# Kernel tuning notes

Measured on AMD Instinct MI355X. Metric: run time of the kernel, lower is better.

## Reference

```python
import jax, jax.numpy as jnp
import numpy as np
from jax import lax

B, CI, CO, H, W = 32, 64, 64, 128, 128
NUM_EXPERTS = 5
NUM_TASKS = 10  # num_tasks=9 + 1 internal global task
K = 5


def setup_inputs() -> dict:
    key = jax.random.key(0)
    ks = jax.random.split(key, 9)
    # kaiming_uniform_ with a=sqrt(5), fan_out -> bound = sqrt(6/((1+5)*fan_out))
    def kaiming(k, co, ci, ksz):
        fan_out = co * ksz * ksz
        bound = np.sqrt(6.0 / (6.0 * fan_out))
        return jax.random.uniform(k, (co, ci, ksz, ksz), jnp.float32, -bound, bound)
    gw_bound = 1.0 / np.sqrt(NUM_TASKS)
    return {
        "x": jax.random.normal(ks[0], (B, CI, H, W), jnp.float32),
        "task_id": jax.random.randint(ks[1], (B,), 0, NUM_TASKS),
        "gate_w": jax.random.uniform(ks[2], (NUM_EXPERTS * CO, NUM_TASKS), jnp.float32, -gw_bound, gw_bound),
        "gate_b": jax.random.uniform(ks[3], (NUM_EXPERTS * CO,), jnp.float32, -gw_bound, gw_bound),
        "w5": kaiming(ks[4], CO, CI, 5),
        "w3": kaiming(ks[5], CO, CI, 3),
        "w1": kaiming(ks[6], CO, CI, 1),
        "wavg3": kaiming(ks[7], CO, CI, 1),
        "wavg5": kaiming(ks[8], CO, CI, 1),
    }


def _expert_bank(w5, w3, w1, wavg3, wavg5):
    # All experts expressed as 5x5 kernels, stacked: [E, O, I, 5, 5]
    pad = lambda w, p: jnp.pad(w, ((0, 0), (0, 0), (p, p), (p, p)))
    avg3 = jnp.full((3, 3), 1.0 / 9.0, w5.dtype)
    avg5 = jnp.full((5, 5), 1.0 / 25.0, w5.dtype)
    e_conv5 = w5
    e_conv3 = pad(w3, 1)
    e_conv1 = pad(w1, 2)
    e_avg3 = pad(wavg3 * avg3[None, None], 1)  # [O,I,1,1]*[3,3] broadcast
    e_avg5 = wavg5 * avg5[None, None]
    return jnp.stack([e_conv5, e_conv3, e_conv1, e_avg3, e_avg5])


def reference(x, task_id, gate_w, gate_b, w5, w3, w1, wavg3, wavg5):
    # Gate: one-hot task -> per-(expert, out_channel) routing weights
    t = jax.nn.one_hot(task_id, NUM_TASKS, dtype=x.dtype)          # [B, T]
    g = t @ gate_w.T + gate_b                                       # [B, E*O]
    g = jax.nn.softmax(g.reshape(-1, NUM_EXPERTS, CO), axis=1)      # [B, E, O]

    experts = _expert_bank(w5, w3, w1, wavg3, wavg5)                # [E, O, I, 5, 5]
    # Batched kernel synthesis (replaces per-sample python loop of einsums)
    w = jnp.einsum('eoikl,beo->boikl', experts, g)                  # [B, O, I, 5, 5]

    # Per-sample conv2d, stride 1, 'same' padding
    def conv1(xi, wi):
        return lax.conv_general_dilated(
            xi[None], wi, (1, 1), 'SAME',
            dimension_numbers=('NCHW', 'OIHW', 'NCHW'))[0]
    y = jax.vmap(conv1)(x, w)                                       # [B, O, H, W]
    # conv_type='final' -> Identity subsequent layer; eval mode -> task_id unchanged
    return y, task_id
```

## Files before the change

kernel.cpp:

```cpp
#include <hip/hip_runtime.h>

#define WK_OFFSET_BYTES 71368704ull

using bf16x8   = __attribute__((ext_vector_type(8)))  __bf16;
using floatx16 = __attribute__((ext_vector_type(16))) float;

static __device__ __forceinline__ unsigned short f2bf(float f) {
    unsigned int u = __float_as_uint(f);
    u += 0x7FFFu + ((u >> 16) & 1u);
    return (unsigned short)(u >> 16);
}

static __device__ __forceinline__ floatx16 mfma16(bf16x8 a, bf16x8 b, floatx16 c) {
    return __builtin_amdgcn_mfma_f32_32x32x16_bf16(a, b, c, 0, 0, 0);
}

static __device__ __forceinline__ void gload_lds16(const void* g, void* l) {
    __builtin_amdgcn_global_load_lds(
        (const __attribute__((address_space(1))) void*)g,
        (__attribute__((address_space(3))) void*)l, 16, 0, 0);
}

__global__ __launch_bounds__(256) void pre_kernel(
    const float* __restrict__ x,
    const float* __restrict__ gate_w, const float* __restrict__ gate_b,
    const float* __restrict__ w5, const float* __restrict__ w3,
    const float* __restrict__ w1, const float* __restrict__ wavg3,
    const float* __restrict__ wavg5, const int* __restrict__ task_id,
    unsigned short* __restrict__ xt, unsigned short* __restrict__ wk,
    float* __restrict__ out_task)
{
    const int blk = blockIdx.x;
    const int tid = threadIdx.x;
    __shared__ float g[5][64];

    if (blk < 4224) {
        const int b  = blk / 132;
        const int hp = blk - b * 132;
        const int h  = hp - 2;
        const bool vrow = (h >= 0) && (h < 128);
        unsigned short* dst_row = xt + (size_t)blk * 8448;

        for (int i = tid; i < 1056; i += 256) {
            int cc = i / 132;
            int wp = i - cc * 132;
            unsigned int pk[4] = {0u, 0u, 0u, 0u};
            if (vrow && wp >= 2 && wp < 130) {
                const float* xp = x + (((size_t)(b * 64 + cc * 8) * 128 + h) * 128 + (wp - 2));
                #pragma unroll
                for (int j = 0; j < 4; ++j) {
                    unsigned short lo = f2bf(xp[(2 * j)     * 16384]);
                    unsigned short hi = f2bf(xp[(2 * j + 1) * 16384]);
                    pk[j] = (unsigned int)lo | ((unsigned int)hi << 16);
                }
            }
            *(uint4*)(dst_row + (size_t)i * 8) = make_uint4(pk[0], pk[1], pk[2], pk[3]);
        }
    } else {
        const int pb = blk - 4224;
        const int t = pb >> 4;
        const int chunk = pb & 15;

        if (tid < 64) {
            float l[5];
            float m = -1e30f;
            #pragma unroll
            for (int e = 0; e < 5; ++e) {
                l[e] = gate_w[(e * 64 + tid) * 10 + t] + gate_b[e * 64 + tid];
                m = fmaxf(m, l[e]);
            }
            float s = 0.f;
            #pragma unroll
            for (int e = 0; e < 5; ++e) { l[e] = expf(l[e] - m); s += l[e]; }
            float inv = 1.f / s;
            #pragma unroll
            for (int e = 0; e < 5; ++e) g[e][tid] = l[e] * inv;
        }
        __syncthreads();

        for (int it = 0; it < 25; ++it) {
            int idx = chunk * 6400 + it * 256 + tid;
            int ci  = idx & 63;
            int o   = (idx >> 6) & 63;
            int tap = idx >> 12;
            int ky = tap / 5, kx = tap - ky * 5;

            float v = g[0][o] * w5[(o * 64 + ci) * 25 + tap];
            bool in3 = (ky >= 1 && ky <= 3 && kx >= 1 && kx <= 3);
            if (in3) {
                v += g[1][o] * w3[(o * 64 + ci) * 9 + (ky - 1) * 3 + (kx - 1)];
                v += g[3][o] * wavg3[o * 64 + ci] * (1.f / 9.f);
            }
            if (ky == 2 && kx == 2) v += g[2][o] * w1[o * 64 + ci];
            v += g[4][o] * wavg5[o * 64 + ci] * (1.f / 25.f);

            wk[(t * 25 + tap) * 4096 + o * 64 + ci] = f2bf(v);
        }

        if (pb == 0 && tid < 32) out_task[tid] = (float)task_id[tid];
    }
}

__global__ __launch_bounds__(512, 2) void conv_kernel(
    const unsigned short* __restrict__ xt, const unsigned short* __restrict__ wk,
    const int* __restrict__ task_id, float* __restrict__ out)
{
    __shared__ unsigned short ibuf[2][25344];
    __shared__ unsigned short wlds[25600];

    const int blk = ((blockIdx.x & 7) << 6) | (blockIdx.x >> 3);
    const int b  = blk >> 4;
    const int ht = blk & 15;
    const int t  = task_id[b];

    const int tid  = threadIdx.x;
    const int lane = tid & 63;
    const int wave = tid >> 6;
    const int rg = wave >> 2;
    const int wc = wave & 3;
    const int lane31 = lane & 31;
    const int laneh  = lane >> 5;

    floatx16 acc[4][2];
    #pragma unroll
    for (int o = 0; o < 4; ++o)
        #pragma unroll
        for (int c = 0; c < 2; ++c)
            #pragma unroll
            for (int r = 0; r < 16; ++r) acc[o][c][r] = 0.f;

    const unsigned short* wkt = wk + t * 102400;
    const size_t ibase0 = ((size_t)(b * 132 + ht * 8)) * 8448;

    auto stage_i = [&](int s, int q) {
        const unsigned short* gsrc = xt + ibase0 + q * 2112;
        unsigned short* ldst = &ibuf[s][0];
        #pragma unroll
        for (int j = 0; j < 6; ++j) {
            int i = j * 512 + tid;
            int r = i / 264;
            int rem = i - r * 264;
            gload_lds16(gsrc + (size_t)r * 8448 + rem * 8, ldst + i * 8);
        }
        if (tid < 96) {
            int i = 3072 + tid;
            int r = i / 264;
            int rem = i - r * 264;
            gload_lds16(gsrc + (size_t)r * 8448 + rem * 8, ldst + i * 8);
        }
    };
    auto stage_w = [&](int q) {
        const unsigned short* gsrc = wkt + q * 16;
        unsigned short* ldst = &wlds[0];
        #pragma unroll
        for (int j = 0; j < 6; ++j) {
            int i = j * 512 + tid;
            int tap = i >> 7;
            int rem = i & 127;
            int cih = rem >> 6;
            int co  = rem & 63;
            gload_lds16(gsrc + tap * 4096 + co * 64 + cih * 8, ldst + i * 8);
        }
        if (tid < 128) {
            int i = 3072 + tid;
            int tap = i >> 7;
            int rem = i & 127;
            int cih = rem >> 6;
            int co  = rem & 63;
            gload_lds16(gsrc + tap * 4096 + co * 64 + cih * 8, ldst + i * 8);
        }
    };

    stage_w(0);
    stage_i(0, 0);
    asm volatile("s_waitcnt vmcnt(0)" ::: "memory");
    __builtin_amdgcn_s_barrier();
    __builtin_amdgcn_sched_barrier(0);

    for (int q = 0; q < 4; ++q) {
        const int s = q & 1;
        if (q < 3) stage_i(s ^ 1, q + 1);

        const unsigned short* ib = &ibuf[s][0];
        __builtin_amdgcn_s_setprio(1);
        #pragma unroll
        for (int kx = 0; kx < 5; ++kx) {
            bf16x8 aF[5][2];
            #pragma unroll
            for (int ky = 0; ky < 5; ++ky) {
                const unsigned short* ap =
                    wlds + (ky * 5 + kx) * 1024 + laneh * 512 + lane31 * 8;
                aF[ky][0] = *(const bf16x8*)(ap);
                aF[ky][1] = *(const bf16x8*)(ap + 256);
            }
            #pragma unroll
            for (int hr = 0; hr < 8; ++hr) {
                const unsigned short* bp =
                    ib + (rg * 4 + hr) * 2112 + laneh * 1056
                       + (wc * 32 + lane31 + kx) * 8;
                bf16x8 bb = *(const bf16x8*)bp;
                #pragma unroll
                for (int ky = 0; ky < 5; ++ky) {
                    const int o = hr - ky;
                    if (o >= 0 && o < 4) {
                        acc[o][0] = mfma16(aF[ky][0], bb, acc[o][0]);
                        acc[o][1] = mfma16(aF[ky][1], bb, acc[o][1]);
                    }
                }
            }
        }
        __builtin_amdgcn_s_setprio(0);

        asm volatile("s_waitcnt lgkmcnt(0)" ::: "memory");
        __builtin_amdgcn_s_barrier();
        __builtin_amdgcn_sched_barrier(0);
        if (q < 3) {
            stage_w(q + 1);
            asm volatile("s_waitcnt vmcnt(0)" ::: "memory");
            __builtin_amdgcn_s_barrier();
            __builtin_amdgcn_sched_barrier(0);
        }
    }

    #pragma unroll
    for (int o = 0; o < 4; ++o) {
        const int h = ht * 8 + rg * 4 + o;
        #pragma unroll
        for (int c = 0; c < 2; ++c) {
            const int w = wc * 32 + lane31;
            #pragma unroll
            for (int reg = 0; reg < 16; ++reg) {
                int co = c * 32 + (reg & 3) + 8 * (reg >> 2) + 4 * laneh;
                out[((size_t)(b * 64 + co) * 128 + h) * 128 + w] = acc[o][c][reg];
            }
        }
    }
}

extern "C" void kernel_launch(void* const* d_in, const int* in_sizes, int n_in,
                              void* d_out, int out_size, void* d_ws, size_t ws_size,
                              hipStream_t stream) {
    const float* x       = (const float*)d_in[0];
    const int*   task_id = (const int*)  d_in[1];
    const float* gate_w  = (const float*)d_in[2];
    const float* gate_b  = (const float*)d_in[3];
    const float* w5      = (const float*)d_in[4];
    const float* w3      = (const float*)d_in[5];
    const float* w1      = (const float*)d_in[6];
    const float* wavg3   = (const float*)d_in[7];
    const float* wavg5   = (const float*)d_in[8];

    float* out = (float*)d_out;
    float* out_task = out + 32 * 64 * 128 * 128;

    unsigned short* xt = (unsigned short*)d_ws;
    unsigned short* wk = (unsigned short*)((char*)d_ws + WK_OFFSET_BYTES);

    pre_kernel<<<dim3(4384), dim3(256), 0, stream>>>(
        x, gate_w, gate_b, w5, w3, w1, wavg3, wavg5, task_id, xt, wk, out_task);
    conv_kernel<<<dim3(512), dim3(512), 0, stream>>>(xt, wk, task_id, out);
}
```

Measured before the change: 351.0 us.

## Read conv weights directly from global memory and halve block row tile

The weight tile is no longer staged into LDS. Each wave now loads its MFMA A-fragments straight from global or L2 memory, which removes the weight staging and the extra barrier in every channel chunk. Blocks shrink to 256 threads covering 4 output rows, with twice as many blocks, and the input double buffer shrinks to match. In exchange, every wave issues strided global weight loads inside the inner loop, and overlapping rows between neighbouring tiles are reloaded more often.

```diff
diff --git a/kernel.cpp b/kernel.cpp
--- a/kernel.cpp
+++ b/kernel.cpp
@@ -101,23 +101,20 @@
     }
 }
 
-__global__ __launch_bounds__(512, 2) void conv_kernel(
+__global__ __launch_bounds__(256, 2) void conv_kernel(
     const unsigned short* __restrict__ xt, const unsigned short* __restrict__ wk,
     const int* __restrict__ task_id, float* __restrict__ out)
 {
-    __shared__ unsigned short ibuf[2][25344];
-    __shared__ unsigned short wlds[25600];
-
-    const int blk = ((blockIdx.x & 7) << 6) | (blockIdx.x >> 3);
-    const int b  = blk >> 4;
-    const int ht = blk & 15;
+    __shared__ unsigned short ibuf[2][16896];
+
+    const int blk = ((blockIdx.x & 7) << 7) | (blockIdx.x >> 3);
+    const int b  = blk >> 5;
+    const int ht = blk & 31;
     const int t  = task_id[b];
 
     const int tid  = threadIdx.x;
     const int lane = tid & 63;
-    const int wave = tid >> 6;
-    const int rg = wave >> 2;
-    const int wc = wave & 3;
+    const int wc   = tid >> 6;
     const int lane31 = lane & 31;
     const int laneh  = lane >> 5;
 
@@ -130,48 +127,26 @@
             for (int r = 0; r < 16; ++r) acc[o][c][r] = 0.f;
 
     const unsigned short* wkt = wk + t * 102400;
-    const size_t ibase0 = ((size_t)(b * 132 + ht * 8)) * 8448;
+    const size_t ibase0 = ((size_t)(b * 132 + ht * 4)) * 8448;
 
     auto stage_i = [&](int s, int q) {
         const unsigned short* gsrc = xt + ibase0 + q * 2112;
         unsigned short* ldst = &ibuf[s][0];
         #pragma unroll
-        for (int j = 0; j < 6; ++j) {
-            int i = j * 512 + tid;
+        for (int j = 0; j < 8; ++j) {
+            int i = j * 256 + tid;
             int r = i / 264;
             int rem = i - r * 264;
             gload_lds16(gsrc + (size_t)r * 8448 + rem * 8, ldst + i * 8);
         }
-        if (tid < 96) {
-            int i = 3072 + tid;
+        if (tid < 64) {
+            int i = 2048 + tid;
             int r = i / 264;
             int rem = i - r * 264;
             gload_lds16(gsrc + (size_t)r * 8448 + rem * 8, ldst + i * 8);
         }
     };
-    auto stage_w = [&](int q) {
-        const unsigned short* gsrc = wkt + q * 16;
-        unsigned short* ldst = &wlds[0];
-        #pragma unroll
-        for (int j = 0; j < 6; ++j) {
-            int i = j * 512 + tid;
-            int tap = i >> 7;
-            int rem = i & 127;
-            int cih = rem >> 6;
-            int co  = rem & 63;
-            gload_lds16(gsrc + tap * 4096 + co * 64 + cih * 8, ldst + i * 8);
-        }
-        if (tid < 128) {
-            int i = 3072 + tid;
-            int tap = i >> 7;
-            int rem = i & 127;
-            int cih = rem >> 6;
-            int co  = rem & 63;
-            gload_lds16(gsrc + tap * 4096 + co * 64 + cih * 8, ldst + i * 8);
-        }
-    };
-
-    stage_w(0);
+
     stage_i(0, 0);
     asm volatile("s_waitcnt vmcnt(0)" ::: "memory");
     __builtin_amdgcn_s_barrier();
@@ -182,23 +157,21 @@
         if (q < 3) stage_i(s ^ 1, q + 1);
 
         const unsigned short* ib = &ibuf[s][0];
+        const unsigned short* wq = wkt + q * 16 + laneh * 8;
         __builtin_amdgcn_s_setprio(1);
         #pragma unroll
         for (int kx = 0; kx < 5; ++kx) {
             bf16x8 aF[5][2];
             #pragma unroll
             for (int ky = 0; ky < 5; ++ky) {
-                const unsigned short* ap =
-                    wlds + (ky * 5 + kx) * 1024 + laneh * 512 + lane31 * 8;
+                const unsigned short* ap = wq + (ky * 5 + kx) * 4096 + lane31 * 64;
                 aF[ky][0] = *(const bf16x8*)(ap);
-                aF[ky][1] = *(const bf16x8*)(ap + 256);
+                aF[ky][1] = *(const bf16x8*)(ap + 2048);
             }
             #pragma unroll
             for (int hr = 0; hr < 8; ++hr) {
-                const unsigned short* bp =
-                    ib + (rg * 4 + hr) * 2112 + laneh * 1056
-                       + (wc * 32 + lane31 + kx) * 8;
-                bf16x8 bb = *(const bf16x8*)bp;
+                bf16x8 bb = *(const bf16x8*)(ib + hr * 2112 + laneh * 1056
+                                             + (wc * 32 + lane31 + kx) * 8);
                 #pragma unroll
                 for (int ky = 0; ky < 5; ++ky) {
                     const int o = hr - ky;
@@ -211,12 +184,8 @@
         }
         __builtin_amdgcn_s_setprio(0);
 
-        asm volatile("s_waitcnt lgkmcnt(0)" ::: "memory");
-        __builtin_amdgcn_s_barrier();
-        __builtin_amdgcn_sched_barrier(0);
         if (q < 3) {
-            stage_w(q + 1);
-            asm volatile("s_waitcnt vmcnt(0)" ::: "memory");
+            asm volatile("s_waitcnt vmcnt(0) lgkmcnt(0)" ::: "memory");
             __builtin_amdgcn_s_barrier();
             __builtin_amdgcn_sched_barrier(0);
         }
@@ -224,7 +193,7 @@
 
     #pragma unroll
     for (int o = 0; o < 4; ++o) {
-        const int h = ht * 8 + rg * 4 + o;
+        const int h = ht * 4 + o;
         #pragma unroll
         for (int c = 0; c < 2; ++c) {
             const int w = wc * 32 + lane31;
@@ -258,5 +227,5 @@
 
     pre_kernel<<<dim3(4384), dim3(256), 0, stream>>>(
         x, gate_w, gate_b, w5, w3, w1, wavg3, wavg5, task_id, xt, wk, out_task);
-    conv_kernel<<<dim3(512), dim3(512), 0, stream>>>(xt, wk, task_id, out);
-}
+    conv_kernel<<<dim3(1024), dim3(256), 0, stream>>>(xt, wk, task_id, out);
+}
```

Result: slower. 369.8 us (+5.4%).

## Prefetch next weight chunk into registers during compute and stagger kx per wave

Applied to the files above, without the earlier changes.

The next weight chunk used to be DMA'd into LDS only after the compute barrier, which stalled the block. It is now loaded from global memory into registers at the start of each iteration, overlapping with the MFMA work, and written to LDS after the barrier. Each wave also starts the kx loop at a different offset, aiming to spread LDS bank accesses across waves. The cost is 28 extra VGPRs per thread for the prefetched data, which may lower occupancy or cause spills in an already register-heavy kernel.

```diff
diff --git a/kernel.cpp b/kernel.cpp
--- a/kernel.cpp
+++ b/kernel.cpp
@@ -120,6 +120,7 @@
     const int wc = wave & 3;
     const int lane31 = lane & 31;
     const int laneh  = lane >> 5;
+    const int kx0 = (wave * 3) % 5;
 
     floatx16 acc[4][2];
     #pragma unroll
@@ -149,29 +150,34 @@
             gload_lds16(gsrc + (size_t)r * 8448 + rem * 8, ldst + i * 8);
         }
     };
-    auto stage_w = [&](int q) {
+    auto stage_w_dma = [&](int q) {
         const unsigned short* gsrc = wkt + q * 16;
         unsigned short* ldst = &wlds[0];
         #pragma unroll
-        for (int j = 0; j < 6; ++j) {
-            int i = j * 512 + tid;
-            int tap = i >> 7;
-            int rem = i & 127;
-            int cih = rem >> 6;
-            int co  = rem & 63;
-            gload_lds16(gsrc + tap * 4096 + co * 64 + cih * 8, ldst + i * 8);
-        }
-        if (tid < 128) {
-            int i = 3072 + tid;
-            int tap = i >> 7;
-            int rem = i & 127;
-            int cih = rem >> 6;
-            int co  = rem & 63;
-            gload_lds16(gsrc + tap * 4096 + co * 64 + cih * 8, ldst + i * 8);
+        for (int j = 0; j < 7; ++j) {
+            if (j < 6 || tid < 128) {
+                int i = j * 512 + tid;
+                int tap = i >> 7;
+                int rem = i & 127;
+                int cih = rem >> 6;
+                int co  = rem & 63;
+                gload_lds16(gsrc + tap * 4096 + co * 64 + cih * 8, ldst + i * 8);
+            }
         }
     };
 
-    stage_w(0);
+    int woff[7];
+    #pragma unroll
+    for (int j = 0; j < 7; ++j) {
+        int i = j * 512 + tid;
+        int tap = i >> 7;
+        int rem = i & 127;
+        int cih = rem >> 6;
+        int co  = rem & 63;
+        woff[j] = tap * 4096 + co * 64 + cih * 8;
+    }
+
+    stage_w_dma(0);
     stage_i(0, 0);
     asm volatile("s_waitcnt vmcnt(0)" ::: "memory");
     __builtin_amdgcn_s_barrier();
@@ -179,26 +185,33 @@
 
     for (int q = 0; q < 4; ++q) {
         const int s = q & 1;
-        if (q < 3) stage_i(s ^ 1, q + 1);
+        uint4 wreg[7] = {};
+        if (q < 3) {
+            stage_i(s ^ 1, q + 1);
+            const unsigned short* wsrc = wkt + (q + 1) * 16;
+            #pragma unroll
+            for (int j = 0; j < 7; ++j)
+                if (j < 6 || tid < 128)
+                    wreg[j] = *(const uint4*)(wsrc + woff[j]);
+        }
 
         const unsigned short* ib = &ibuf[s][0];
         __builtin_amdgcn_s_setprio(1);
         #pragma unroll
-        for (int kx = 0; kx < 5; ++kx) {
+        for (int kk = 0; kk < 5; ++kk) {
+            int kx = kk + kx0; if (kx >= 5) kx -= 5;
+            const unsigned short* wkx = wlds + kx * 1024 + laneh * 512 + lane31 * 8;
+            const unsigned short* ibb = ib + laneh * 1056 + (wc * 32 + lane31 + kx) * 8;
             bf16x8 aF[5][2];
             #pragma unroll
             for (int ky = 0; ky < 5; ++ky) {
-                const unsigned short* ap =
-                    wlds + (ky * 5 + kx) * 1024 + laneh * 512 + lane31 * 8;
+                const unsigned short* ap = wkx + ky * 5120;
                 aF[ky][0] = *(const bf16x8*)(ap);
                 aF[ky][1] = *(const bf16x8*)(ap + 256);
             }
             #pragma unroll
             for (int hr = 0; hr < 8; ++hr) {
-                const unsigned short* bp =
-                    ib + (rg * 4 + hr) * 2112 + laneh * 1056
-                       + (wc * 32 + lane31 + kx) * 8;
-                bf16x8 bb = *(const bf16x8*)bp;
+                bf16x8 bb = *(const bf16x8*)(ibb + (rg * 4 + hr) * 2112);
                 #pragma unroll
                 for (int ky = 0; ky < 5; ++ky) {
                     const int o = hr - ky;
@@ -215,8 +228,12 @@
         __builtin_amdgcn_s_barrier();
         __builtin_amdgcn_sched_barrier(0);
         if (q < 3) {
-            stage_w(q + 1);
             asm volatile("s_waitcnt vmcnt(0)" ::: "memory");
+            #pragma unroll
+            for (int j = 0; j < 7; ++j)
+                if (j < 6 || tid < 128)
+                    *(uint4*)(wlds + (j * 512 + tid) * 8) = wreg[j];
+            asm volatile("s_waitcnt lgkmcnt(0)" ::: "memory");
             __builtin_amdgcn_s_barrier();
             __builtin_amdgcn_sched_barrier(0);
         }
```

Result: slower. 364.8 us (+4.0%).
